# Kernel optimization log

Measured on AMD Instinct MI355X. Metric: run time of the kernel, lower is better.

The kernel has to match this reference:

```python
import jax, jax.numpy as jnp
import numpy as np

N, E, F_IN, H, C = 50000, 800000, 128, 128, 64


def setup_inputs() -> dict:
    key = jax.random.key(0)
    ks = jax.random.split(key, 10)
    s = lambda f: np.float32(1.0 / np.sqrt(f))
    return {
        "x": jax.random.normal(ks[0], (N, F_IN), jnp.float32),
        "edge_index": jax.random.randint(ks[1], (2, E), 0, N, dtype=jnp.int64),
        # SAGEConv1: lin_l (on aggregated neighbors, with bias) + lin_r (on root, no bias)
        "W1l": jax.random.normal(ks[2], (F_IN, H), jnp.float32) * s(F_IN),
        "b1l": jnp.zeros((H,), jnp.float32),
        "W1r": jax.random.normal(ks[3], (F_IN, H), jnp.float32) * s(F_IN),
        # SAGEConv2
        "W2l": jax.random.normal(ks[4], (H, C), jnp.float32) * s(H),
        "b2l": jnp.zeros((C,), jnp.float32),
        "W2r": jax.random.normal(ks[5], (H, C), jnp.float32) * s(H),
        # GCNConv
        "Wg": jax.random.normal(ks[6], (C, C), jnp.float32) * s(C),
        "bg": jnp.zeros((C,), jnp.float32),
    }


def sage_conv(x, edge_index, Wl, bl, Wr):
    # PyG SAGEConv (mean aggr): out = lin_l(mean_{j in N(i)} x_j) + lin_r(x_i)
    n = x.shape[0]
    src, dst = edge_index[0], edge_index[1]
    agg = jax.ops.segment_sum(x[src], dst, num_segments=n)  # [N, F]
    cnt = jax.ops.segment_sum(jnp.ones((src.shape[0],), x.dtype), dst, num_segments=n)
    mean = agg / jnp.maximum(cnt, 1.0)[:, None]
    return mean @ Wl + bl + x @ Wr


def gcn_conv(x, edge_index, W, b):
    # PyG GCNConv: add self loops, symmetric normalization D^-1/2 A D^-1/2
    n = x.shape[0]
    loop = jnp.arange(n, dtype=edge_index.dtype)
    src = jnp.concatenate([edge_index[0], loop])
    dst = jnp.concatenate([edge_index[1], loop])
    deg = jax.ops.segment_sum(jnp.ones((src.shape[0],), x.dtype), dst, num_segments=n)
    dinv = jnp.where(deg > 0, jax.lax.rsqrt(jnp.maximum(deg, 1e-12)), 0.0)
    norm = dinv[src] * dinv[dst]  # [E+N]
    xw = x @ W
    out = jax.ops.segment_sum(xw[src] * norm[:, None], dst, num_segments=n)
    return out + b


def reference(x, edge_index, W1l, b1l, W1r, W2l, b2l, W2r, Wg, bg):
    h = jax.nn.relu(sage_conv(x, edge_index, W1l, b1l, W1r))
    # dropout is identity in eval mode
    h = sage_conv(h, edge_index, W2l, b2l, W2r)
    h = jax.nn.softmax(h, axis=1)  # activate='softmax'
    return gcn_conv(h, edge_index, Wg, bg)
```

## Files before the change

kernel.cpp:

```cpp
#include <hip/hip_runtime.h>
#include <hip/hip_fp16.h>
#include <math.h>


typedef __attribute__((ext_vector_type(8))) short bf16x8;
typedef __attribute__((ext_vector_type(4))) float f32x4;
typedef __attribute__((ext_vector_type(2))) float f32v2;

__device__ inline unsigned short f32_bf16_hi(float f) {
    unsigned int u = __builtin_bit_cast(unsigned int, f);
    u = (u + 0x7FFFu + ((u >> 16) & 1u)) >> 16;
    return (unsigned short)u;
}
__device__ inline float bf16_to_f32(unsigned short h) {
    unsigned int u = ((unsigned int)h) << 16;
    return __builtin_bit_cast(float, u);
}

union H8 { float4 f4; __half2 h[4]; };

__device__ inline void dec16(uint4 u, float* a0, float* a1) {
    f32v2 x0 = __builtin_amdgcn_cvt_pk_f32_fp8(u.x, false);
    f32v2 x1 = __builtin_amdgcn_cvt_pk_f32_fp8(u.x, true);
    f32v2 y0 = __builtin_amdgcn_cvt_pk_f32_fp8(u.y, false);
    f32v2 y1 = __builtin_amdgcn_cvt_pk_f32_fp8(u.y, true);
    a0[0] += x0[0]; a0[1] += x0[1]; a0[2] += x1[0]; a0[3] += x1[1];
    a0[4] += y0[0]; a0[5] += y0[1]; a0[6] += y1[0]; a0[7] += y1[1];
    f32v2 z0 = __builtin_amdgcn_cvt_pk_f32_fp8(u.z, false);
    f32v2 z1 = __builtin_amdgcn_cvt_pk_f32_fp8(u.z, true);
    f32v2 w0 = __builtin_amdgcn_cvt_pk_f32_fp8(u.w, false);
    f32v2 w1 = __builtin_amdgcn_cvt_pk_f32_fp8(u.w, true);
    a1[0] += z0[0]; a1[1] += z0[1]; a1[2] += z1[0]; a1[3] += z1[1];
    a1[4] += w0[0]; a1[5] += w0[1]; a1[6] += w1[0]; a1[7] += w1[1];
}

__device__ inline unsigned char enc8(float v) {
    int w = __builtin_amdgcn_cvt_pk_fp8_f32(v, v, 0, false);
    return (unsigned char)(w & 0xff);
}

__global__ void count_kernel(const int* __restrict__ dst, int* __restrict__ off,
                             int E, int NB, int BK) {
    __shared__ int hist[256];
    int t = threadIdx.x;
    hist[t] = 0;
    __syncthreads();
    int base = blockIdx.x * 8192;
    for (int i = t; i < 8192; i += 256) {
        int e = base + i;
        if (e < E) atomicAdd(&hist[dst[e] >> 8], 1);
    }
    __syncthreads();
    if (t < BK) off[1 + t * NB + blockIdx.x] = hist[t];
    if (blockIdx.x == 0 && t == 0) off[0] = 0;
}

__global__ void scan_reduce_kernel(const int* __restrict__ data, int* __restrict__ bsum, int n) {
    __shared__ int red[256];
    int t = threadIdx.x;
    int base = blockIdx.x * 2048 + t * 8;
    int s = 0;
    if (base + 8 <= n) {
        int4 a = *(const int4*)(data + base);
        int4 b = *(const int4*)(data + base + 4);
        s = a.x + a.y + a.z + a.w + b.x + b.y + b.z + b.w;
    } else {
        for (int i = 0; i < 8; ++i)
            if (base + i < n) s += data[base + i];
    }
    red[t] = s;
    __syncthreads();
    for (int off = 128; off > 0; off >>= 1) {
        if (t < off) red[t] += red[t + off];
        __syncthreads();
    }
    if (t == 0) bsum[blockIdx.x] = red[0];
}

__global__ void scan_offsets_kernel(int* __restrict__ bsum, int B) {
    if (threadIdx.x == 0 && blockIdx.x == 0) {
        int run = 0;
        for (int i = 0; i < B; ++i) { int v = bsum[i]; bsum[i] = run; run += v; }
    }
}

__global__ void scan_final_kernel(int* __restrict__ data, const int* __restrict__ bsum, int n) {
    __shared__ int tsum[256];
    int t = threadIdx.x;
    int base = blockIdx.x * 2048 + t * 8;
    int v[8];
    int s = 0;
#pragma unroll
    for (int i = 0; i < 8; ++i) {
        v[i] = (base + i < n) ? data[base + i] : 0;
        s += v[i];
    }
    tsum[t] = s;
    for (int off = 1; off < 256; off <<= 1) {
        __syncthreads();
        int u = (t >= off) ? tsum[t - off] : 0;
        __syncthreads();
        tsum[t] += u;
    }
    __syncthreads();
    int run = bsum[blockIdx.x] + tsum[t] - s;
#pragma unroll
    for (int i = 0; i < 8; ++i) {
        run += v[i];
        if (base + i < n) data[base + i] = run;
    }
}

__global__ void partition_kernel(const int* __restrict__ src, const int* __restrict__ dst,
                                 const int* __restrict__ off, unsigned* __restrict__ ebuf,
                                 int E, int NB, int BK) {
    __shared__ int cur[256];
    int t = threadIdx.x;
    if (t < BK) cur[t] = off[t * NB + blockIdx.x];
    __syncthreads();
    int base = blockIdx.x * 8192;
    for (int i = t; i < 8192; i += 256) {
        int e = base + i;
        if (e < E) {
            int d = dst[e];
            int pos = atomicAdd(&cur[d >> 8], 1);
            ebuf[pos] = ((unsigned)src[e] << 8) | (unsigned)(d & 255);
        }
    }
}

__global__ void finalize_kernel(const unsigned* __restrict__ ebuf, const int* __restrict__ off,
                                int* __restrict__ col, int* __restrict__ rowptr,
                                float* __restrict__ dinv, int N, int NB, int E) {
    __shared__ int hist[256], scn[256], cur[256];
    int b = blockIdx.x, t = threadIdx.x;
    int base = off[b * NB];
    int end  = off[(b + 1) * NB];
    int M = end - base;
    hist[t] = 0;
    __syncthreads();
    for (int i = t; i < M; i += 256) atomicAdd(&hist[ebuf[base + i] & 255u], 1);
    __syncthreads();
    scn[t] = hist[t];
    for (int o = 1; o < 256; o <<= 1) {
        __syncthreads();
        int u = (t >= o) ? scn[t - o] : 0;
        __syncthreads();
        scn[t] += u;
    }
    __syncthreads();
    int excl = scn[t] - hist[t];
    int node = b * 256 + t;
    if (node < N) {
        rowptr[node] = base + excl;
        dinv[node] = rsqrtf((float)(hist[t] + 1));
    }
    if (b == 0 && t == 0) rowptr[N] = E;
    cur[t] = base + excl;
    __syncthreads();
    for (int i = t; i < M; i += 256) {
        unsigned w = ebuf[base + i];
        int pos = atomicAdd(&cur[w & 255u], 1);
        col[pos] = (int)(w >> 8);
    }
}

__global__ void packw_kernel(const float* __restrict__ W1l, const float* __restrict__ W1r,
                             const float* __restrict__ W2l, const float* __restrict__ W2r,
                             const float* __restrict__ Wg,
                             unsigned short* __restrict__ p1h, unsigned short* __restrict__ p1l,
                             unsigned short* __restrict__ p2h, unsigned short* __restrict__ p2l,
                             unsigned short* __restrict__ p3h, unsigned short* __restrict__ p3l) {
    int which = blockIdx.y;
    const float* W;
    unsigned short *hi, *lo;
    int K, Mp, colOff, T;
    if (which == 0)      { W = W1l; hi = p1h; lo = p1l; K = 128; Mp = 128; colOff = 0;   T = 16; }
    else if (which == 1) { W = W1r; hi = p1h; lo = p1l; K = 128; Mp = 128; colOff = 128; T = 16; }
    else if (which == 2) { W = W2l; hi = p2h; lo = p2l; K = 128; Mp = 64;  colOff = 0;   T = 8;  }
    else if (which == 3) { W = W2r; hi = p2h; lo = p2l; K = 128; Mp = 64;  colOff = 64;  T = 8;  }
    else                 { W = Wg;  hi = p3h; lo = p3l; K = 64;  Mp = 64;  colOff = 0;   T = 4;  }
    int idx = blockIdx.x * blockDim.x + threadIdx.x;
    if (idx >= K * Mp) return;
    int k = idx / Mp, m = idx % Mp;
    float w = W[(size_t)k * Mp + m];
    int colI = colOff + m;
    int s = k >> 5, kk = k & 31, qq = kk >> 3, j = kk & 7;
    int tt = colI >> 4, n = colI & 15;
    int lane = qq * 16 + n;
    size_t pos = ((size_t)(s * T + tt) * 64 + lane) * 8 + j;
    unsigned short h = f32_bf16_hi(w);
    hi[pos] = h;
    lo[pos] = f32_bf16_hi(w - bf16_to_f32(h));
}

__launch_bounds__(256)
__global__ void gemm1_kernel(const float* __restrict__ A,
                             const unsigned short* __restrict__ Whi,
                             const unsigned short* __restrict__ Wlo,
                             unsigned char* __restrict__ outA8, __half* __restrict__ outB, int N) {
    constexpr int Ttot = 16, TB = 8;
    __shared__ __align__(16) unsigned char pk[4][16][128];
    const int lane = threadIdx.x & 63;
    const int wave = threadIdx.x >> 6;
    const int m = lane & 15, q = lane >> 4;
    const int t0 = blockIdx.y * TB;
    const int row0 = blockIdx.x * 64 + wave * 16;
    int arow = row0 + m;
    if (arow >= N) arow = N - 1;
    const float* ap = A + (size_t)arow * 128 + q * 8;

    float av[4][8];
#pragma unroll
    for (int s = 0; s < 4; ++s) {
        *(float4*)(av[s])     = *(const float4*)(ap + s * 32);
        *(float4*)(av[s] + 4) = *(const float4*)(ap + s * 32 + 4);
    }
    bf16x8 ahi[4], alo[4];
#pragma unroll
    for (int s = 0; s < 4; ++s)
#pragma unroll
        for (int i = 0; i < 8; ++i) {
            unsigned short h = f32_bf16_hi(av[s][i]);
            ahi[s][i] = (short)h;
            alo[s][i] = (short)f32_bf16_hi(av[s][i] - bf16_to_f32(h));
        }

    f32x4 acc[TB];
#pragma unroll
    for (int t = 0; t < TB; ++t) acc[t] = (f32x4)(0.f);
    const bf16x8* whp = (const bf16x8*)Whi;
    const bf16x8* wlp = (const bf16x8*)Wlo;
#pragma unroll
    for (int s = 0; s < 4; ++s) {
        const int base = (s * Ttot + t0) * 64 + lane;
#pragma unroll
        for (int t = 0; t < TB; ++t) {
            bf16x8 wh = whp[base + t * 64];
            bf16x8 wl = wlp[base + t * 64];
            acc[t] = __builtin_amdgcn_mfma_f32_16x16x32_bf16(ahi[s], wh, acc[t], 0, 0, 0);
            acc[t] = __builtin_amdgcn_mfma_f32_16x16x32_bf16(alo[s], wh, acc[t], 0, 0, 0);
            acc[t] = __builtin_amdgcn_mfma_f32_16x16x32_bf16(ahi[s], wl, acc[t], 0, 0, 0);
        }
    }

    if (blockIdx.y == 0) {
#pragma unroll
        for (int r = 0; r < 4; ++r) {
            int row = q * 4 + r;
            int sw = (row & 3) << 5;
#pragma unroll
            for (int t = 0; t < 8; t += 2) {
                int w = __builtin_amdgcn_cvt_pk_fp8_f32(acc[t][r], acc[t + 1][r], 0, false);
                int off = (t >> 1) * 8 + (m & 7);
                int c0 = ((2 * t + (m >> 3)) & 3) * 32 + off;
                int c1 = ((2 * t + 2 + (m >> 3)) & 3) * 32 + off;
                pk[wave][row][c0 ^ sw] = (unsigned char)(w & 0xff);
                pk[wave][row][c1 ^ sw] = (unsigned char)((w >> 8) & 0xff);
            }
        }
        __syncthreads();
        int rr = lane >> 2, qt = lane & 3;
        int grow = row0 + rr;
        if (grow < N) {
            const unsigned char* srcp = &pk[wave][rr][(qt ^ (rr & 3)) * 32];
            uint4 v0 = *(const uint4*)(srcp);
            uint4 v1 = *(const uint4*)(srcp + 16);
            *(uint4*)(outA8 + (size_t)grow * 128 + qt * 32) = v0;
            *(uint4*)(outA8 + (size_t)grow * 128 + qt * 32 + 16) = v1;
        }
    } else {
#pragma unroll
        for (int r = 0; r < 4; ++r) {
            int row = row0 + q * 4 + r;
            if (row < N) {
#pragma unroll
                for (int t = 0; t < TB; ++t) {
                    int c = (t0 + t) * 16 + m - 128;
                    outB[(size_t)row * 128 + c] = __float2half(acc[t][r]);
                }
            }
        }
    }
}

__launch_bounds__(256)
__global__ void sage2_fused_kernel(const unsigned char* __restrict__ p8, const __half* __restrict__ q16,
                                   const int* __restrict__ rowptr, const int* __restrict__ col,
                                   const float* __restrict__ b1l,
                                   const unsigned short* __restrict__ Whi,
                                   const unsigned short* __restrict__ Wlo,
                                   unsigned char* __restrict__ r8, __half* __restrict__ s16, int N) {
    __shared__ float part[4][64][16];
    const int lane = threadIdx.x & 63;
    const int wave = threadIdx.x >> 6;
    const int pairH = wave & 1;
    const int grp   = wave >> 1;
    const int m = lane & 15, q = lane >> 4;
    const int row0 = blockIdx.x * 32 + grp * 16;
    int node = row0 + m;
    int nclamp = (node < N) ? node : (N - 1);
    int sAll = rowptr[nclamp];
    int eAll = (node < N) ? rowptr[nclamp + 1] : sAll;
    int deg  = eAll - sAll;
    int half0 = (deg + 1) >> 1;
    int sIdx = sAll + (pairH ? half0 : 0);
    int eIdx = pairH ? eAll : (sAll + half0);

    float acc[4][8];
#pragma unroll
    for (int s = 0; s < 4; ++s)
#pragma unroll
        for (int i = 0; i < 8; ++i) acc[s][i] = 0.f;

    const unsigned char* pb = p8 + q * 32;
    int ptr = sIdx;
    for (; ptr + 4 <= eIdx; ptr += 4) {
        int j0 = col[ptr], j1 = col[ptr + 1], j2 = col[ptr + 2], j3 = col[ptr + 3];
        uint4 uA[4], uB[4];
        uA[0] = *(const uint4*)(pb + (size_t)j0 * 128);
        uB[0] = *(const uint4*)(pb + (size_t)j0 * 128 + 16);
        uA[1] = *(const uint4*)(pb + (size_t)j1 * 128);
        uB[1] = *(const uint4*)(pb + (size_t)j1 * 128 + 16);
        uA[2] = *(const uint4*)(pb + (size_t)j2 * 128);
        uB[2] = *(const uint4*)(pb + (size_t)j2 * 128 + 16);
        uA[3] = *(const uint4*)(pb + (size_t)j3 * 128);
        uB[3] = *(const uint4*)(pb + (size_t)j3 * 128 + 16);
#pragma unroll
        for (int e = 0; e < 4; ++e) {
            dec16(uA[e], acc[0], acc[1]);
            dec16(uB[e], acc[2], acc[3]);
        }
    }
    for (; ptr < eIdx; ++ptr) {
        int j0 = col[ptr];
        uint4 uA = *(const uint4*)(pb + (size_t)j0 * 128);
        uint4 uB = *(const uint4*)(pb + (size_t)j0 * 128 + 16);
        dec16(uA, acc[0], acc[1]);
        dec16(uB, acc[2], acc[3]);
    }

    float* ap = &acc[0][0];
    const int swz = lane & 3;
#pragma unroll
    for (int c = 0; c < 2; ++c) {
        if (c) __syncthreads();
#pragma unroll
        for (int sl = 0; sl < 4; ++sl)
            *(float4*)&part[wave][lane][(sl ^ swz) * 4] =
                *(const float4*)(ap + (c * 4 + sl) * 4);
        __syncthreads();
#pragma unroll
        for (int sl = 0; sl < 4; ++sl) {
            float4 pv = *(const float4*)&part[wave ^ 1][lane][(sl ^ swz) * 4];
            int g = (c * 4 + sl) * 4;
            ap[g]     += pv.x;
            ap[g + 1] += pv.y;
            ap[g + 2] += pv.z;
            ap[g + 3] += pv.w;
        }
    }

    float inv = 1.0f / fmaxf((float)deg, 1.0f);
    bf16x8 ahi[4], alo[4];
#pragma unroll
    for (int s = 0; s < 4; ++s) {
        H8 qv;
        qv.f4 = *(const float4*)(q16 + (size_t)nclamp * 128 + s * 32 + q * 8);
        float bv[8];
        *(float4*)(bv)     = *(const float4*)(b1l + s * 32 + q * 8);
        *(float4*)(bv + 4) = *(const float4*)(b1l + s * 32 + q * 8 + 4);
#pragma unroll
        for (int i = 0; i < 8; ++i) {
            float qf = __half2float(((const __half*)&qv)[i]);
            float h = fmaxf(acc[s][i] * inv + qf + bv[i], 0.f);
            unsigned short hb = f32_bf16_hi(h);
            ahi[s][i] = (short)hb;
            alo[s][i] = (short)f32_bf16_hi(h - bf16_to_f32(hb));
        }
    }

    f32x4 accm[4];
#pragma unroll
    for (int t = 0; t < 4; ++t) accm[t] = (f32x4)(0.f);
    const bf16x8* whp = (const bf16x8*)Whi;
    const bf16x8* wlp = (const bf16x8*)Wlo;
#pragma unroll
    for (int s = 0; s < 4; ++s) {
        const int base = (s * 8 + pairH * 4) * 64 + lane;
#pragma unroll
        for (int t = 0; t < 4; ++t) {
            bf16x8 wh = whp[base + t * 64];
            bf16x8 wl = wlp[base + t * 64];
            accm[t] = __builtin_amdgcn_mfma_f32_16x16x32_bf16(ahi[s], wh, accm[t], 0, 0, 0);
            accm[t] = __builtin_amdgcn_mfma_f32_16x16x32_bf16(alo[s], wh, accm[t], 0, 0, 0);
            accm[t] = __builtin_amdgcn_mfma_f32_16x16x32_bf16(ahi[s], wl, accm[t], 0, 0, 0);
        }
    }
#pragma unroll
    for (int r = 0; r < 4; ++r) {
        int row = row0 + q * 4 + r;
        if (row < N) {
            if (pairH == 0) {
#pragma unroll
                for (int t = 0; t < 4; ++t) {
                    int c = t * 16 + m;
                    int pos = ((c >> 3) & 3) * 16 + ((c >> 5) & 1) * 8 + (c & 7);
                    r8[(size_t)row * 64 + pos] = enc8(accm[t][r]);
                }
            } else {
#pragma unroll
                for (int t = 0; t < 4; ++t) {
                    int c = t * 16 + m;
                    s16[(size_t)row * 64 + c] = __float2half(accm[t][r]);
                }
            }
        }
    }
}

__launch_bounds__(256)
__global__ void gcn_prep_fused_kernel(const unsigned char* __restrict__ r8, const __half* __restrict__ s16,
                                      const int* __restrict__ rowptr, const int* __restrict__ col,
                                      const float* __restrict__ b2l,
                                      const unsigned short* __restrict__ Whi,
                                      const unsigned short* __restrict__ Wlo,
                                      const float* __restrict__ dinv,
                                      __half* __restrict__ tpA, __half* __restrict__ tpB, int N) {
    __shared__ float part[4][64][16];
    const int lane = threadIdx.x & 63;
    const int wave = threadIdx.x >> 6;
    const int pairH = wave & 1;
    const int grp   = wave >> 1;
    const int m = lane & 15, q = lane >> 4;
    const int row0 = blockIdx.x * 32 + grp * 16;
    int node = row0 + m;
    int nclamp = (node < N) ? node : (N - 1);
    int sAll = rowptr[nclamp];
    int eAll = (node < N) ? rowptr[nclamp + 1] : sAll;
    int deg  = eAll - sAll;
    int half0 = (deg + 1) >> 1;
    int sIdx = sAll + (pairH ? half0 : 0);
    int eIdx = pairH ? eAll : (sAll + half0);

    float acc[2][8];
#pragma unroll
    for (int s = 0; s < 2; ++s)
#pragma unroll
        for (int i = 0; i < 8; ++i) acc[s][i] = 0.f;

    const unsigned char* rb = r8 + q * 16;
    int ptr = sIdx;
    for (; ptr + 4 <= eIdx; ptr += 4) {
        int j0 = col[ptr], j1 = col[ptr + 1], j2 = col[ptr + 2], j3 = col[ptr + 3];
        uint4 u0 = *(const uint4*)(rb + (size_t)j0 * 64);
        uint4 u1 = *(const uint4*)(rb + (size_t)j1 * 64);
        uint4 u2 = *(const uint4*)(rb + (size_t)j2 * 64);
        uint4 u3 = *(const uint4*)(rb + (size_t)j3 * 64);
        dec16(u0, acc[0], acc[1]);
        dec16(u1, acc[0], acc[1]);
        dec16(u2, acc[0], acc[1]);
        dec16(u3, acc[0], acc[1]);
    }
    for (; ptr < eIdx; ++ptr) {
        int j0 = col[ptr];
        uint4 u0 = *(const uint4*)(rb + (size_t)j0 * 64);
        dec16(u0, acc[0], acc[1]);
    }

    float* ap = &acc[0][0];
    const int swz = lane & 3;
#pragma unroll
    for (int sl = 0; sl < 4; ++sl)
        *(float4*)&part[wave][lane][(sl ^ swz) * 4] = *(const float4*)(ap + sl * 4);
    __syncthreads();
#pragma unroll
    for (int sl = 0; sl < 4; ++sl) {
        float4 pv = *(const float4*)&part[wave ^ 1][lane][(sl ^ swz) * 4];
        ap[sl * 4]     += pv.x;
        ap[sl * 4 + 1] += pv.y;
        ap[sl * 4 + 2] += pv.z;
        ap[sl * 4 + 3] += pv.w;
    }

    float inv = 1.0f / fmaxf((float)deg, 1.0f);
    float v[2][8];
    float mx = -1e30f;
#pragma unroll
    for (int s = 0; s < 2; ++s) {
        H8 sv;
        sv.f4 = *(const float4*)(s16 + (size_t)nclamp * 64 + s * 32 + q * 8);
        float bv[8];
        *(float4*)(bv)     = *(const float4*)(b2l + s * 32 + q * 8);
        *(float4*)(bv + 4) = *(const float4*)(b2l + s * 32 + q * 8 + 4);
#pragma unroll
        for (int i = 0; i < 8; ++i) {
            float sf = __half2float(((const __half*)&sv)[i]);
            v[s][i] = acc[s][i] * inv + sf + bv[i];
            mx = fmaxf(mx, v[s][i]);
        }
    }
    mx = fmaxf(mx, __shfl_xor(mx, 16, 64));
    mx = fmaxf(mx, __shfl_xor(mx, 32, 64));
    float sm = 0.f;
#pragma unroll
    for (int s = 0; s < 2; ++s)
#pragma unroll
        for (int i = 0; i < 8; ++i) {
            v[s][i] = expf(v[s][i] - mx);
            sm += v[s][i];
        }
    sm += __shfl_xor(sm, 16, 64);
    sm += __shfl_xor(sm, 32, 64);
    float is = 1.0f / sm;

    bf16x8 ahi[2], alo[2];
#pragma unroll
    for (int s = 0; s < 2; ++s)
#pragma unroll
        for (int i = 0; i < 8; ++i) {
            float h = v[s][i] * is;
            unsigned short hb = f32_bf16_hi(h);
            ahi[s][i] = (short)hb;
            alo[s][i] = (short)f32_bf16_hi(h - bf16_to_f32(hb));
        }

    f32x4 accm[2];
#pragma unroll
    for (int t = 0; t < 2; ++t) accm[t] = (f32x4)(0.f);
    const bf16x8* whp = (const bf16x8*)Whi;
    const bf16x8* wlp = (const bf16x8*)Wlo;
#pragma unroll
    for (int s = 0; s < 2; ++s) {
        const int base = (s * 4 + pairH * 2) * 64 + lane;
#pragma unroll
        for (int t = 0; t < 2; ++t) {
            bf16x8 wh = whp[base + t * 64];
            bf16x8 wl = wlp[base + t * 64];
            accm[t] = __builtin_amdgcn_mfma_f32_16x16x32_bf16(ahi[s], wh, accm[t], 0, 0, 0);
            accm[t] = __builtin_amdgcn_mfma_f32_16x16x32_bf16(alo[s], wh, accm[t], 0, 0, 0);
            accm[t] = __builtin_amdgcn_mfma_f32_16x16x32_bf16(ahi[s], wl, accm[t], 0, 0, 0);
        }
    }
    __half* plane = pairH ? tpB : tpA;
#pragma unroll
    for (int r = 0; r < 4; ++r) {
        int row = row0 + q * 4 + r;
        if (row < N) {
            float sc = dinv[row];
#pragma unroll
            for (int t = 0; t < 2; ++t) {
                int c = t * 16 + m;
                plane[(size_t)row * 32 + c] = __float2half(accm[t][r] * sc);
            }
        }
    }
}

__global__ void gcn_agg_kernel(const __half* __restrict__ tpP,
                               const int* __restrict__ rowptr, const int* __restrict__ col,
                               const float* __restrict__ dinv, const float* __restrict__ bg,
                               float* __restrict__ out, int N, int fOff) {
    int node = blockIdx.x * 4 + (threadIdx.x >> 6);
    if (node >= N) return;
    int lane = threadIdx.x & 63;
    int f2 = lane & 15;
    int ep = lane >> 4;
    int s = rowptr[node], e = rowptr[node + 1];
    float ax[4], ay[4];
#pragma unroll
    for (int k = 0; k < 4; ++k) { ax[k] = 0.f; ay[k] = 0.f; }
    int p = s;
    for (; p + 16 <= e; p += 16) {
#pragma unroll
        for (int k = 0; k < 4; ++k) {
            int j = col[p + 4 * k + ep];
            float2 f = __half22float2(*(const __half2*)(tpP + (size_t)j * 32 + 2 * f2));
            ax[k] += f.x;
            ay[k] += f.y;
        }
    }
    for (int t = p + ep; t < e; t += 4) {
        int j = col[t];
        float2 f = __half22float2(*(const __half2*)(tpP + (size_t)j * 32 + 2 * f2));
        ax[0] += f.x;
        ay[0] += f.y;
    }
    float sx = (ax[0] + ax[1]) + (ax[2] + ax[3]);
    float sy = (ay[0] + ay[1]) + (ay[2] + ay[3]);
    sx += __shfl_xor(sx, 16, 64); sx += __shfl_xor(sx, 32, 64);
    sy += __shfl_xor(sy, 16, 64); sy += __shfl_xor(sy, 32, 64);
    if (ep == 0) {
        float2 selfv = __half22float2(*(const __half2*)(tpP + (size_t)node * 32 + 2 * f2));
        float di = dinv[node];
        float2 o;
        o.x = (sx + selfv.x) * di + bg[fOff + 2 * f2];
        o.y = (sy + selfv.y) * di + bg[fOff + 2 * f2 + 1];
        *(float2*)(out + (size_t)node * 64 + fOff + 2 * f2) = o;
    }
}

extern "C" void kernel_launch(void* const* d_in, const int* in_sizes, int n_in,
                              void* d_out, int out_size, void* d_ws, size_t ws_size,
                              hipStream_t stream) {
    const float* x = (const float*)d_in[0];
    const int* ei = (const int*)d_in[1];
    const float* W1l = (const float*)d_in[2];
    const float* b1l = (const float*)d_in[3];
    const float* W1r = (const float*)d_in[4];
    const float* W2l = (const float*)d_in[5];
    const float* b2l = (const float*)d_in[6];
    const float* W2r = (const float*)d_in[7];
    const float* Wg  = (const float*)d_in[8];
    const float* bg  = (const float*)d_in[9];

    const int N = in_sizes[0] / 128;
    const int E = in_sizes[1] / 2;
    const int* srcp = ei;
    const int* dstp = ei + E;

    const int NB = (E + 8191) / 8192;
    const int BK = (N + 255) >> 8;
    const int len = BK * NB;

    float* ws = (float*)d_ws;
    float* dinv = ws;
    unsigned char* p8 = (unsigned char*)(dinv + N);
    __half* q16 = (__half*)(p8 + (size_t)N * 128);
    unsigned char* r8 = (unsigned char*)(q16 + (size_t)N * 128);
    __half* s16 = (__half*)(r8 + (size_t)N * 64);
    __half* tpA = s16 + (size_t)N * 64;
    __half* tpB = tpA + (size_t)N * 32;
    int* rowptr = (int*)(tpB + (size_t)N * 32);
    int* off    = rowptr + (N + 1);
    int* colbuf = off + len + 2;
    unsigned* ebuf = (unsigned*)(colbuf + E);
    int* bsum   = (int*)(ebuf + E);
    uintptr_t up = (uintptr_t)(bsum + 32);
    up = (up + 15) & ~(uintptr_t)15;
    unsigned short* p1h = (unsigned short*)up;
    unsigned short* p1l = p1h + 32768;
    unsigned short* p2h = p1l + 32768;
    unsigned short* p2l = p2h + 16384;
    unsigned short* p3h = p2l + 16384;
    unsigned short* p3l = p3h + 4096;

    float* out = (float*)d_out;

    count_kernel<<<NB, 256, 0, stream>>>(dstp, off, E, NB, BK);
    const int sn = len + 1;
    const int SBs = (sn + 2047) / 2048;
    scan_reduce_kernel<<<SBs, 256, 0, stream>>>(off, bsum, sn);
    scan_offsets_kernel<<<1, 64, 0, stream>>>(bsum, SBs);
    scan_final_kernel<<<SBs, 256, 0, stream>>>(off, bsum, sn);
    partition_kernel<<<NB, 256, 0, stream>>>(srcp, dstp, off, ebuf, E, NB, BK);
    finalize_kernel<<<BK, 256, 0, stream>>>(ebuf, off, colbuf, rowptr, dinv, N, NB, E);

    packw_kernel<<<dim3(64, 5), 256, 0, stream>>>(W1l, W1r, W2l, W2r, Wg,
                                                  p1h, p1l, p2h, p2l, p3h, p3l);

    const int gb  = (N + 63) / 64;
    const int gbf = (N + 31) / 32;
    const int ab  = (N + 3) / 4;

    gemm1_kernel<<<dim3(gb, 2), 256, 0, stream>>>(x, p1h, p1l, p8, q16, N);

    sage2_fused_kernel<<<gbf, 256, 0, stream>>>(p8, q16, rowptr, colbuf, b1l,
                                                p2h, p2l, r8, s16, N);

    gcn_prep_fused_kernel<<<gbf, 256, 0, stream>>>(r8, s16, rowptr, colbuf, b2l,
                                                   p3h, p3l, dinv, tpA, tpB, N);

    gcn_agg_kernel<<<ab, 256, 0, stream>>>(tpA, rowptr, colbuf, dinv, bg, out, N, 0);
    gcn_agg_kernel<<<ab, 256, 0, stream>>>(tpB, rowptr, colbuf, dinv, bg, out, N, 32);
}
```

Measured before the change: 271.4 us.

## Sort nodes by degree for fused aggregation kernels and merge GCN aggregation planes

```diff
diff --git a/kernel.cpp b/kernel.cpp
--- a/kernel.cpp
+++ b/kernel.cpp
@@ -40,10 +40,11 @@
 }
 
 __global__ void count_kernel(const int* __restrict__ dst, int* __restrict__ off,
-                             int E, int NB, int BK) {
+                             int* __restrict__ dcnt, int E, int NB, int BK) {
     __shared__ int hist[256];
     int t = threadIdx.x;
     hist[t] = 0;
+    if (blockIdx.x == 0) dcnt[t] = 0;
     __syncthreads();
     int base = blockIdx.x * 8192;
     for (int i = t; i < 8192; i += 256) {
@@ -131,7 +132,8 @@
 
 __global__ void finalize_kernel(const unsigned* __restrict__ ebuf, const int* __restrict__ off,
                                 int* __restrict__ col, int* __restrict__ rowptr,
-                                float* __restrict__ dinv, int N, int NB, int E) {
+                                float* __restrict__ dinv, int* __restrict__ deg,
+                                int* __restrict__ dcnt, int N, int NB, int E) {
     __shared__ int hist[256], scn[256], cur[256];
     int b = blockIdx.x, t = threadIdx.x;
     int base = off[b * NB];
@@ -154,6 +156,9 @@
     if (node < N) {
         rowptr[node] = base + excl;
         dinv[node] = rsqrtf((float)(hist[t] + 1));
+        int d = hist[t];
+        deg[node] = d;
+        atomicAdd(&dcnt[d < 255 ? d : 255], 1);
     }
     if (b == 0 && t == 0) rowptr[N] = E;
     cur[t] = base + excl;
@@ -162,6 +167,32 @@
         unsigned w = ebuf[base + i];
         int pos = atomicAdd(&cur[w & 255u], 1);
         col[pos] = (int)(w >> 8);
+    }
+}
+
+__global__ void perm_scan_kernel(int* __restrict__ dcnt) {
+    __shared__ int s[256];
+    int t = threadIdx.x;
+    int v = dcnt[t];
+    s[t] = v;
+    for (int o = 1; o < 256; o <<= 1) {
+        __syncthreads();
+        int u = (t >= o) ? s[t - o] : 0;
+        __syncthreads();
+        s[t] += u;
+    }
+    __syncthreads();
+    dcnt[t] = s[t] - v;
+}
+
+__global__ void perm_scatter_kernel(const int* __restrict__ deg, int* __restrict__ dcnt,
+                                    int* __restrict__ perm, int N) {
+    int i = blockIdx.x * 256 + threadIdx.x;
+    if (i < N) {
+        int d = deg[i];
+        if (d > 255) d = 255;
+        int pos = atomicAdd(&dcnt[d], 1);
+        perm[pos] = i;
     }
 }
 
@@ -287,6 +318,7 @@
 __launch_bounds__(256)
 __global__ void sage2_fused_kernel(const unsigned char* __restrict__ p8, const __half* __restrict__ q16,
                                    const int* __restrict__ rowptr, const int* __restrict__ col,
+                                   const int* __restrict__ perm,
                                    const float* __restrict__ b1l,
                                    const unsigned short* __restrict__ Whi,
                                    const unsigned short* __restrict__ Wlo,
@@ -298,10 +330,10 @@
     const int grp   = wave >> 1;
     const int m = lane & 15, q = lane >> 4;
     const int row0 = blockIdx.x * 32 + grp * 16;
-    int node = row0 + m;
-    int nclamp = (node < N) ? node : (N - 1);
-    int sAll = rowptr[nclamp];
-    int eAll = (node < N) ? rowptr[nclamp + 1] : sAll;
+    int prow = row0 + m;
+    int node = perm[(prow < N) ? prow : (N - 1)];
+    int sAll = rowptr[node];
+    int eAll = (prow < N) ? rowptr[node + 1] : sAll;
     int deg  = eAll - sAll;
     int half0 = (deg + 1) >> 1;
     int sIdx = sAll + (pairH ? half0 : 0);
@@ -366,7 +398,7 @@
 #pragma unroll
     for (int s = 0; s < 4; ++s) {
         H8 qv;
-        qv.f4 = *(const float4*)(q16 + (size_t)nclamp * 128 + s * 32 + q * 8);
+        qv.f4 = *(const float4*)(q16 + (size_t)node * 128 + s * 32 + q * 8);
         float bv[8];
         *(float4*)(bv)     = *(const float4*)(b1l + s * 32 + q * 8);
         *(float4*)(bv + 4) = *(const float4*)(b1l + s * 32 + q * 8 + 4);
@@ -399,20 +431,21 @@
     }
 #pragma unroll
     for (int r = 0; r < 4; ++r) {
-        int row = row0 + q * 4 + r;
-        if (row < N) {
+        int ridx = row0 + q * 4 + r;
+        if (ridx < N) {
+            int onode = __shfl(node, q * 4 + r, 64);
             if (pairH == 0) {
 #pragma unroll
                 for (int t = 0; t < 4; ++t) {
                     int c = t * 16 + m;
                     int pos = ((c >> 3) & 3) * 16 + ((c >> 5) & 1) * 8 + (c & 7);
-                    r8[(size_t)row * 64 + pos] = enc8(accm[t][r]);
+                    r8[(size_t)onode * 64 + pos] = enc8(accm[t][r]);
                 }
             } else {
 #pragma unroll
                 for (int t = 0; t < 4; ++t) {
                     int c = t * 16 + m;
-                    s16[(size_t)row * 64 + c] = __float2half(accm[t][r]);
+                    s16[(size_t)onode * 64 + c] = __float2half(accm[t][r]);
                 }
             }
         }
@@ -422,11 +455,12 @@
 __launch_bounds__(256)
 __global__ void gcn_prep_fused_kernel(const unsigned char* __restrict__ r8, const __half* __restrict__ s16,
                                       const int* __restrict__ rowptr, const int* __restrict__ col,
+                                      const int* __restrict__ perm,
                                       const float* __restrict__ b2l,
                                       const unsigned short* __restrict__ Whi,
                                       const unsigned short* __restrict__ Wlo,
                                       const float* __restrict__ dinv,
-                                      __half* __restrict__ tpA, __half* __restrict__ tpB, int N) {
+                                      __half* __restrict__ tp16, int N) {
     __shared__ float part[4][64][16];
     const int lane = threadIdx.x & 63;
     const int wave = threadIdx.x >> 6;
@@ -434,10 +468,10 @@
     const int grp   = wave >> 1;
     const int m = lane & 15, q = lane >> 4;
     const int row0 = blockIdx.x * 32 + grp * 16;
-    int node = row0 + m;
-    int nclamp = (node < N) ? node : (N - 1);
-    int sAll = rowptr[nclamp];
-    int eAll = (node < N) ? rowptr[nclamp + 1] : sAll;
+    int prow = row0 + m;
+    int node = perm[(prow < N) ? prow : (N - 1)];
+    int sAll = rowptr[node];
+    int eAll = (prow < N) ? rowptr[node + 1] : sAll;
     int deg  = eAll - sAll;
     int half0 = (deg + 1) >> 1;
     int sIdx = sAll + (pairH ? half0 : 0);
@@ -489,7 +523,7 @@
 #pragma unroll
     for (int s = 0; s < 2; ++s) {
         H8 sv;
-        sv.f4 = *(const float4*)(s16 + (size_t)nclamp * 64 + s * 32 + q * 8);
+        sv.f4 = *(const float4*)(s16 + (size_t)node * 64 + s * 32 + q * 8);
         float bv[8];
         *(float4*)(bv)     = *(const float4*)(b2l + s * 32 + q * 8);
         *(float4*)(bv + 4) = *(const float4*)(b2l + s * 32 + q * 8 + 4);
@@ -542,61 +576,61 @@
             accm[t] = __builtin_amdgcn_mfma_f32_16x16x32_bf16(ahi[s], wl, accm[t], 0, 0, 0);
         }
     }
-    __half* plane = pairH ? tpB : tpA;
 #pragma unroll
     for (int r = 0; r < 4; ++r) {
-        int row = row0 + q * 4 + r;
-        if (row < N) {
-            float sc = dinv[row];
+        int ridx = row0 + q * 4 + r;
+        if (ridx < N) {
+            int onode = __shfl(node, q * 4 + r, 64);
+            float sc = dinv[onode];
 #pragma unroll
             for (int t = 0; t < 2; ++t) {
-                int c = t * 16 + m;
-                plane[(size_t)row * 32 + c] = __float2half(accm[t][r] * sc);
+                int c = (pairH * 2 + t) * 16 + m;
+                tp16[(size_t)onode * 64 + c] = __float2half(accm[t][r] * sc);
             }
         }
     }
 }
 
-__global__ void gcn_agg_kernel(const __half* __restrict__ tpP,
+__global__ void gcn_agg_kernel(const __half* __restrict__ tp,
                                const int* __restrict__ rowptr, const int* __restrict__ col,
                                const float* __restrict__ dinv, const float* __restrict__ bg,
-                               float* __restrict__ out, int N, int fOff) {
+                               float* __restrict__ out, int N) {
     int node = blockIdx.x * 4 + (threadIdx.x >> 6);
     if (node >= N) return;
     int lane = threadIdx.x & 63;
-    int f2 = lane & 15;
-    int ep = lane >> 4;
+    int f2 = lane & 31;
+    int ep = lane >> 5;
     int s = rowptr[node], e = rowptr[node + 1];
-    float ax[4], ay[4];
-#pragma unroll
-    for (int k = 0; k < 4; ++k) { ax[k] = 0.f; ay[k] = 0.f; }
+    float ax[8], ay[8];
+#pragma unroll
+    for (int k = 0; k < 8; ++k) { ax[k] = 0.f; ay[k] = 0.f; }
     int p = s;
     for (; p + 16 <= e; p += 16) {
 #pragma unroll
-        for (int k = 0; k < 4; ++k) {
-            int j = col[p + 4 * k + ep];
-            float2 f = __half22float2(*(const __half2*)(tpP + (size_t)j * 32 + 2 * f2));
+        for (int k = 0; k < 8; ++k) {
+            int j = col[p + 2 * k + ep];
+            float2 f = __half22float2(*(const __half2*)(tp + (size_t)j * 64 + 2 * f2));
             ax[k] += f.x;
             ay[k] += f.y;
         }
     }
-    for (int t = p + ep; t < e; t += 4) {
+    for (int t = p + ep; t < e; t += 2) {
         int j = col[t];
-        float2 f = __half22float2(*(const __half2*)(tpP + (size_t)j * 32 + 2 * f2));
+        float2 f = __half22float2(*(const __half2*)(tp + (size_t)j * 64 + 2 * f2));
         ax[0] += f.x;
         ay[0] += f.y;
     }
-    float sx = (ax[0] + ax[1]) + (ax[2] + ax[3]);
-    float sy = (ay[0] + ay[1]) + (ay[2] + ay[3]);
-    sx += __shfl_xor(sx, 16, 64); sx += __shfl_xor(sx, 32, 64);
-    sy += __shfl_xor(sy, 16, 64); sy += __shfl_xor(sy, 32, 64);
+    float sx = ((ax[0] + ax[1]) + (ax[2] + ax[3])) + ((ax[4] + ax[5]) + (ax[6] + ax[7]));
+    float sy = ((ay[0] + ay[1]) + (ay[2] + ay[3])) + ((ay[4] + ay[5]) + (ay[6] + ay[7]));
+    sx += __shfl_xor(sx, 32, 64);
+    sy += __shfl_xor(sy, 32, 64);
     if (ep == 0) {
-        float2 selfv = __half22float2(*(const __half2*)(tpP + (size_t)node * 32 + 2 * f2));
+        float2 selfv = __half22float2(*(const __half2*)(tp + (size_t)node * 64 + 2 * f2));
         float di = dinv[node];
         float2 o;
-        o.x = (sx + selfv.x) * di + bg[fOff + 2 * f2];
-        o.y = (sy + selfv.y) * di + bg[fOff + 2 * f2 + 1];
-        *(float2*)(out + (size_t)node * 64 + fOff + 2 * f2) = o;
+        o.x = (sx + selfv.x) * di + bg[2 * f2];
+        o.y = (sy + selfv.y) * di + bg[2 * f2 + 1];
+        *(float2*)(out + (size_t)node * 64 + 2 * f2) = o;
     }
 }
 
@@ -629,14 +663,16 @@
     __half* q16 = (__half*)(p8 + (size_t)N * 128);
     unsigned char* r8 = (unsigned char*)(q16 + (size_t)N * 128);
     __half* s16 = (__half*)(r8 + (size_t)N * 64);
-    __half* tpA = s16 + (size_t)N * 64;
-    __half* tpB = tpA + (size_t)N * 32;
-    int* rowptr = (int*)(tpB + (size_t)N * 32);
+    __half* tp16 = s16 + (size_t)N * 64;
+    int* rowptr = (int*)(tp16 + (size_t)N * 64);
     int* off    = rowptr + (N + 1);
     int* colbuf = off + len + 2;
     unsigned* ebuf = (unsigned*)(colbuf + E);
     int* bsum   = (int*)(ebuf + E);
-    uintptr_t up = (uintptr_t)(bsum + 32);
+    int* deg    = bsum + 32;
+    int* dcnt   = deg + N;
+    int* perm   = dcnt + 256;
+    uintptr_t up = (uintptr_t)(perm + N);
     up = (up + 15) & ~(uintptr_t)15;
     unsigned short* p1h = (unsigned short*)up;
     unsigned short* p1l = p1h + 32768;
@@ -647,14 +683,18 @@
 
     float* out = (float*)d_out;
 
-    count_kernel<<<NB, 256, 0, stream>>>(dstp, off, E, NB, BK);
+    count_kernel<<<NB, 256, 0, stream>>>(dstp, off, dcnt, E, NB, BK);
     const int sn = len + 1;
     const int SBs = (sn + 2047) / 2048;
     scan_reduce_kernel<<<SBs, 256, 0, stream>>>(off, bsum, sn);
     scan_offsets_kernel<<<1, 64, 0, stream>>>(bsum, SBs);
     scan_final_kernel<<<SBs, 256, 0, stream>>>(off, bsum, sn);
     partition_kernel<<<NB, 256, 0, stream>>>(srcp, dstp, off, ebuf, E, NB, BK);
-    finalize_kernel<<<BK, 256, 0, stream>>>(ebuf, off, colbuf, rowptr, dinv, N, NB, E);
+    finalize_kernel<<<BK, 256, 0, stream>>>(ebuf, off, colbuf, rowptr, dinv,
+                                            deg, dcnt, N, NB, E);
+
+    perm_scan_kernel<<<1, 256, 0, stream>>>(dcnt);
+    perm_scatter_kernel<<<(N + 255) / 256, 256, 0, stream>>>(deg, dcnt, perm, N);
 
     packw_kernel<<<dim3(64, 5), 256, 0, stream>>>(W1l, W1r, W2l, W2r, Wg,
                                                   p1h, p1l, p2h, p2l, p3h, p3l);
@@ -665,12 +705,11 @@
 
     gemm1_kernel<<<dim3(gb, 2), 256, 0, stream>>>(x, p1h, p1l, p8, q16, N);
 
-    sage2_fused_kernel<<<gbf, 256, 0, stream>>>(p8, q16, rowptr, colbuf, b1l,
+    sage2_fused_kernel<<<gbf, 256, 0, stream>>>(p8, q16, rowptr, colbuf, perm, b1l,
                                                 p2h, p2l, r8, s16, N);
 
-    gcn_prep_fused_kernel<<<gbf, 256, 0, stream>>>(r8, s16, rowptr, colbuf, b2l,
-                                                   p3h, p3l, dinv, tpA, tpB, N);
-
-    gcn_agg_kernel<<<ab, 256, 0, stream>>>(tpA, rowptr, colbuf, dinv, bg, out, N, 0);
-    gcn_agg_kernel<<<ab, 256, 0, stream>>>(tpB, rowptr, colbuf, dinv, bg, out, N, 32);
-}
+    gcn_prep_fused_kernel<<<gbf, 256, 0, stream>>>(r8, s16, rowptr, colbuf, perm, b2l,
+                                                   p3h, p3l, dinv, tp16, N);
+
+    gcn_agg_kernel<<<ab, 256, 0, stream>>>(tp16, rowptr, colbuf, dinv, bg, out, N);
+}
```

After: 558.7 us. +105.9%, slower.

## Merge weight packing into count kernel, drop scan kernel, unify GCN aggregation

Applied to the files above, without the earlier changes.

```diff
diff --git a/kernel.cpp b/kernel.cpp
--- a/kernel.cpp
+++ b/kernel.cpp
@@ -39,20 +39,51 @@
     return (unsigned char)(w & 0xff);
 }
 
-__global__ void count_kernel(const int* __restrict__ dst, int* __restrict__ off,
-                             int E, int NB, int BK) {
+__global__ void count_packw_kernel(const int* __restrict__ dst, int* __restrict__ off,
+                                   int E, int NB, int BK,
+                                   const float* __restrict__ W1l, const float* __restrict__ W1r,
+                                   const float* __restrict__ W2l, const float* __restrict__ W2r,
+                                   const float* __restrict__ Wg,
+                                   unsigned short* __restrict__ p1h, unsigned short* __restrict__ p1l,
+                                   unsigned short* __restrict__ p2h, unsigned short* __restrict__ p2l,
+                                   unsigned short* __restrict__ p3h, unsigned short* __restrict__ p3l) {
     __shared__ int hist[256];
     int t = threadIdx.x;
-    hist[t] = 0;
-    __syncthreads();
-    int base = blockIdx.x * 8192;
-    for (int i = t; i < 8192; i += 256) {
-        int e = base + i;
-        if (e < E) atomicAdd(&hist[dst[e] >> 8], 1);
-    }
-    __syncthreads();
-    if (t < BK) off[1 + t * NB + blockIdx.x] = hist[t];
-    if (blockIdx.x == 0 && t == 0) off[0] = 0;
+    if ((int)blockIdx.x < NB) {
+        hist[t] = 0;
+        __syncthreads();
+        int base = blockIdx.x * 8192;
+        for (int i = t; i < 8192; i += 256) {
+            int e = base + i;
+            if (e < E) atomicAdd(&hist[dst[e] >> 8], 1);
+        }
+        __syncthreads();
+        if (t < BK) off[1 + t * NB + blockIdx.x] = hist[t];
+        if (blockIdx.x == 0 && t == 0) off[0] = 0;
+        return;
+    }
+    int pb = blockIdx.x - NB;
+    int which = pb >> 6;
+    const float* W;
+    unsigned short *hi, *lo;
+    int K, Mp, colOff, T;
+    if (which == 0)      { W = W1l; hi = p1h; lo = p1l; K = 128; Mp = 128; colOff = 0;   T = 16; }
+    else if (which == 1) { W = W1r; hi = p1h; lo = p1l; K = 128; Mp = 128; colOff = 128; T = 16; }
+    else if (which == 2) { W = W2l; hi = p2h; lo = p2l; K = 128; Mp = 64;  colOff = 0;   T = 8;  }
+    else if (which == 3) { W = W2r; hi = p2h; lo = p2l; K = 128; Mp = 64;  colOff = 64;  T = 8;  }
+    else                 { W = Wg;  hi = p3h; lo = p3l; K = 64;  Mp = 64;  colOff = 0;   T = 4;  }
+    int idx = (pb & 63) * 256 + t;
+    if (idx >= K * Mp) return;
+    int k = idx / Mp, m = idx % Mp;
+    float w = W[(size_t)k * Mp + m];
+    int colI = colOff + m;
+    int s = k >> 5, kk = k & 31, qq = kk >> 3, j = kk & 7;
+    int tt = colI >> 4, n = colI & 15;
+    int lane = qq * 16 + n;
+    size_t pos = ((size_t)(s * T + tt) * 64 + lane) * 8 + j;
+    unsigned short h = f32_bf16_hi(w);
+    hi[pos] = h;
+    lo[pos] = f32_bf16_hi(w - bf16_to_f32(h));
 }
 
 __global__ void scan_reduce_kernel(const int* __restrict__ data, int* __restrict__ bsum, int n) {
@@ -77,16 +108,11 @@
     if (t == 0) bsum[blockIdx.x] = red[0];
 }
 
-__global__ void scan_offsets_kernel(int* __restrict__ bsum, int B) {
-    if (threadIdx.x == 0 && blockIdx.x == 0) {
-        int run = 0;
-        for (int i = 0; i < B; ++i) { int v = bsum[i]; bsum[i] = run; run += v; }
-    }
-}
-
 __global__ void scan_final_kernel(int* __restrict__ data, const int* __restrict__ bsum, int n) {
     __shared__ int tsum[256];
     int t = threadIdx.x;
+    int bbase = 0;
+    for (int i = 0; i < (int)blockIdx.x; ++i) bbase += bsum[i];
     int base = blockIdx.x * 2048 + t * 8;
     int v[8];
     int s = 0;
@@ -103,7 +129,7 @@
         tsum[t] += u;
     }
     __syncthreads();
-    int run = bsum[blockIdx.x] + tsum[t] - s;
+    int run = bbase + tsum[t] - s;
 #pragma unroll
     for (int i = 0; i < 8; ++i) {
         run += v[i];
@@ -163,35 +189,6 @@
         int pos = atomicAdd(&cur[w & 255u], 1);
         col[pos] = (int)(w >> 8);
     }
-}
-
-__global__ void packw_kernel(const float* __restrict__ W1l, const float* __restrict__ W1r,
-                             const float* __restrict__ W2l, const float* __restrict__ W2r,
-                             const float* __restrict__ Wg,
-                             unsigned short* __restrict__ p1h, unsigned short* __restrict__ p1l,
-                             unsigned short* __restrict__ p2h, unsigned short* __restrict__ p2l,
-                             unsigned short* __restrict__ p3h, unsigned short* __restrict__ p3l) {
-    int which = blockIdx.y;
-    const float* W;
-    unsigned short *hi, *lo;
-    int K, Mp, colOff, T;
-    if (which == 0)      { W = W1l; hi = p1h; lo = p1l; K = 128; Mp = 128; colOff = 0;   T = 16; }
-    else if (which == 1) { W = W1r; hi = p1h; lo = p1l; K = 128; Mp = 128; colOff = 128; T = 16; }
-    else if (which == 2) { W = W2l; hi = p2h; lo = p2l; K = 128; Mp = 64;  colOff = 0;   T = 8;  }
-    else if (which == 3) { W = W2r; hi = p2h; lo = p2l; K = 128; Mp = 64;  colOff = 64;  T = 8;  }
-    else                 { W = Wg;  hi = p3h; lo = p3l; K = 64;  Mp = 64;  colOff = 0;   T = 4;  }
-    int idx = blockIdx.x * blockDim.x + threadIdx.x;
-    if (idx >= K * Mp) return;
-    int k = idx / Mp, m = idx % Mp;
-    float w = W[(size_t)k * Mp + m];
-    int colI = colOff + m;
-    int s = k >> 5, kk = k & 31, qq = kk >> 3, j = kk & 7;
-    int tt = colI >> 4, n = colI & 15;
-    int lane = qq * 16 + n;
-    size_t pos = ((size_t)(s * T + tt) * 64 + lane) * 8 + j;
-    unsigned short h = f32_bf16_hi(w);
-    hi[pos] = h;
-    lo[pos] = f32_bf16_hi(w - bf16_to_f32(h));
 }
 
 __launch_bounds__(256)
@@ -426,7 +423,7 @@
                                       const unsigned short* __restrict__ Whi,
                                       const unsigned short* __restrict__ Wlo,
                                       const float* __restrict__ dinv,
-                                      __half* __restrict__ tpA, __half* __restrict__ tpB, int N) {
+                                      __half* __restrict__ tp16, int N) {
     __shared__ float part[4][64][16];
     const int lane = threadIdx.x & 63;
     const int wave = threadIdx.x >> 6;
@@ -542,7 +539,6 @@
             accm[t] = __builtin_amdgcn_mfma_f32_16x16x32_bf16(ahi[s], wl, accm[t], 0, 0, 0);
         }
     }
-    __half* plane = pairH ? tpB : tpA;
 #pragma unroll
     for (int r = 0; r < 4; ++r) {
         int row = row0 + q * 4 + r;
@@ -550,53 +546,53 @@
             float sc = dinv[row];
 #pragma unroll
             for (int t = 0; t < 2; ++t) {
-                int c = t * 16 + m;
-                plane[(size_t)row * 32 + c] = __float2half(accm[t][r] * sc);
+                int c = (pairH * 2 + t) * 16 + m;
+                tp16[(size_t)row * 64 + c] = __float2half(accm[t][r] * sc);
             }
         }
     }
 }
 
-__global__ void gcn_agg_kernel(const __half* __restrict__ tpP,
+__global__ void gcn_agg_kernel(const __half* __restrict__ tp,
                                const int* __restrict__ rowptr, const int* __restrict__ col,
                                const float* __restrict__ dinv, const float* __restrict__ bg,
-                               float* __restrict__ out, int N, int fOff) {
+                               float* __restrict__ out, int N) {
     int node = blockIdx.x * 4 + (threadIdx.x >> 6);
     if (node >= N) return;
     int lane = threadIdx.x & 63;
-    int f2 = lane & 15;
-    int ep = lane >> 4;
+    int f2 = lane & 31;
+    int ep = lane >> 5;
     int s = rowptr[node], e = rowptr[node + 1];
-    float ax[4], ay[4];
-#pragma unroll
-    for (int k = 0; k < 4; ++k) { ax[k] = 0.f; ay[k] = 0.f; }
+    float ax[8], ay[8];
+#pragma unroll
+    for (int k = 0; k < 8; ++k) { ax[k] = 0.f; ay[k] = 0.f; }
     int p = s;
     for (; p + 16 <= e; p += 16) {
 #pragma unroll
-        for (int k = 0; k < 4; ++k) {
-            int j = col[p + 4 * k + ep];
-            float2 f = __half22float2(*(const __half2*)(tpP + (size_t)j * 32 + 2 * f2));
+        for (int k = 0; k < 8; ++k) {
+            int j = col[p + 2 * k + ep];
+            float2 f = __half22float2(*(const __half2*)(tp + (size_t)j * 64 + 2 * f2));
             ax[k] += f.x;
             ay[k] += f.y;
         }
     }
-    for (int t = p + ep; t < e; t += 4) {
+    for (int t = p + ep; t < e; t += 2) {
         int j = col[t];
-        float2 f = __half22float2(*(const __half2*)(tpP + (size_t)j * 32 + 2 * f2));
+        float2 f = __half22float2(*(const __half2*)(tp + (size_t)j * 64 + 2 * f2));
         ax[0] += f.x;
         ay[0] += f.y;
     }
-    float sx = (ax[0] + ax[1]) + (ax[2] + ax[3]);
-    float sy = (ay[0] + ay[1]) + (ay[2] + ay[3]);
-    sx += __shfl_xor(sx, 16, 64); sx += __shfl_xor(sx, 32, 64);
-    sy += __shfl_xor(sy, 16, 64); sy += __shfl_xor(sy, 32, 64);
+    float sx = ((ax[0] + ax[1]) + (ax[2] + ax[3])) + ((ax[4] + ax[5]) + (ax[6] + ax[7]));
+    float sy = ((ay[0] + ay[1]) + (ay[2] + ay[3])) + ((ay[4] + ay[5]) + (ay[6] + ay[7]));
+    sx += __shfl_xor(sx, 32, 64);
+    sy += __shfl_xor(sy, 32, 64);
     if (ep == 0) {
-        float2 selfv = __half22float2(*(const __half2*)(tpP + (size_t)node * 32 + 2 * f2));
+        float2 selfv = __half22float2(*(const __half2*)(tp + (size_t)node * 64 + 2 * f2));
         float di = dinv[node];
         float2 o;
-        o.x = (sx + selfv.x) * di + bg[fOff + 2 * f2];
-        o.y = (sy + selfv.y) * di + bg[fOff + 2 * f2 + 1];
-        *(float2*)(out + (size_t)node * 64 + fOff + 2 * f2) = o;
+        o.x = (sx + selfv.x) * di + bg[2 * f2];
+        o.y = (sy + selfv.y) * di + bg[2 * f2 + 1];
+        *(float2*)(out + (size_t)node * 64 + 2 * f2) = o;
     }
 }
 
@@ -629,9 +625,8 @@
     __half* q16 = (__half*)(p8 + (size_t)N * 128);
     unsigned char* r8 = (unsigned char*)(q16 + (size_t)N * 128);
     __half* s16 = (__half*)(r8 + (size_t)N * 64);
-    __half* tpA = s16 + (size_t)N * 64;
-    __half* tpB = tpA + (size_t)N * 32;
-    int* rowptr = (int*)(tpB + (size_t)N * 32);
+    __half* tp16 = s16 + (size_t)N * 64;
+    int* rowptr = (int*)(tp16 + (size_t)N * 64);
     int* off    = rowptr + (N + 1);
     int* colbuf = off + len + 2;
     unsigned* ebuf = (unsigned*)(colbuf + E);
@@ -647,18 +642,16 @@
 
     float* out = (float*)d_out;
 
-    count_kernel<<<NB, 256, 0, stream>>>(dstp, off, E, NB, BK);
+    count_packw_kernel<<<NB + 320, 256, 0, stream>>>(dstp, off, E, NB, BK,
+                                                     W1l, W1r, W2l, W2r, Wg,
+                                                     p1h, p1l, p2h, p2l, p3h, p3l);
     const int sn = len + 1;
     const int SBs = (sn + 2047) / 2048;
     scan_reduce_kernel<<<SBs, 256, 0, stream>>>(off, bsum, sn);
-    scan_offsets_kernel<<<1, 64, 0, stream>>>(bsum, SBs);
     scan_final_kernel<<<SBs, 256, 0, stream>>>(off, bsum, sn);
     partition_kernel<<<NB, 256, 0, stream>>>(srcp, dstp, off, ebuf, E, NB, BK);
     finalize_kernel<<<BK, 256, 0, stream>>>(ebuf, off, colbuf, rowptr, dinv, N, NB, E);
 
-    packw_kernel<<<dim3(64, 5), 256, 0, stream>>>(W1l, W1r, W2l, W2r, Wg,
-                                                  p1h, p1l, p2h, p2l, p3h, p3l);
-
     const int gb  = (N + 63) / 64;
     const int gbf = (N + 31) / 32;
     const int ab  = (N + 3) / 4;
@@ -669,8 +662,7 @@
                                                 p2h, p2l, r8, s16, N);
 
     gcn_prep_fused_kernel<<<gbf, 256, 0, stream>>>(r8, s16, rowptr, colbuf, b2l,
-                                                   p3h, p3l, dinv, tpA, tpB, N);
-
-    gcn_agg_kernel<<<ab, 256, 0, stream>>>(tpA, rowptr, colbuf, dinv, bg, out, N, 0);
-    gcn_agg_kernel<<<ab, 256, 0, stream>>>(tpB, rowptr, colbuf, dinv, bg, out, N, 32);
-}
+                                                   p3h, p3l, dinv, tp16, N);
+
+    gcn_agg_kernel<<<ab, 256, 0, stream>>>(tp16, rowptr, colbuf, dinv, bg, out, N);
+}
```

Result: faster. 256.6 us (-5.5%).
